# Kernel optimization log

Measured on AMD Instinct MI355X. Metric: run time of the kernel, lower is better.

## Reference

```python
import jax, jax.numpy as jnp
import numpy as np

BEV_H, BEV_W = 496, 432  # cfg.bevshape

def mish(x):
    return x * jnp.tanh(jax.nn.softplus(x))

def ln(x, g, b, eps=1e-5):
    m = jnp.mean(x, axis=-1, keepdims=True)
    v = jnp.mean((x - m) ** 2, axis=-1, keepdims=True)
    return (x - m) * jax.lax.rsqrt(v + eps) * g + b

def fel(x, W, g, b):
    # FELayer: Linear(bias=False) -> LayerNorm -> Mish
    return mish(ln(x @ W.T, g, b))

def setup_inputs() -> dict:
    key = jax.random.key(0)
    ks = iter(jax.random.split(key, 48))
    Nv, P, Cin, Cv, Nb = 16000, 32, 10, 64, 16000
    inp = {}
    inp['voxels'] = jax.random.normal(next(ks), (Nv, P, Cin), jnp.float32)
    inp['voxelmask'] = jax.random.bernoulli(next(ks), 0.7, (Nv, P, 1)).astype(jnp.float32)
    inp['bevsidx'] = jax.random.randint(next(ks), (Nb, 64), 0, Nv, dtype=jnp.int32)
    flat = jax.random.choice(next(ks), BEV_H * BEV_W, (Nb,), replace=False)
    inp['bevcoors'] = jnp.stack([flat // BEV_W, flat % BEV_W], axis=1).astype(jnp.int32)
    inp['bevmask'] = jax.random.bernoulli(next(ks), 0.8, (Nb, 1, 1)).astype(jnp.float32)
    def w(shape):
        return jax.random.normal(next(ks), shape, jnp.float32) * 0.05
    for i, cin in zip((1, 2, 3, 4), (Cin, Cv, Cv, Cv)):
        inp[f'vfe{i}_W'] = w((Cv, cin))
        inp[f'vfe{i}_g'] = jnp.ones((Cv,), jnp.float32)
        inp[f'vfe{i}_b'] = jnp.zeros((Cv,), jnp.float32)
    inp['bfe1_W'] = w((16, Cv, Cv));  inp['bfe1_g'] = jnp.ones((16, Cv));  inp['bfe1_b'] = jnp.zeros((16, Cv))
    inp['bfe2a_W'] = w((16, 8, Cv)); inp['bfe2a_g'] = jnp.ones((16, 8));  inp['bfe2a_b'] = jnp.zeros((16, 8))
    inp['bfe2b_W'] = w((16, 8, 32)); inp['bfe2b_g'] = jnp.ones((16, 8));  inp['bfe2b_b'] = jnp.zeros((16, 8))
    inp['bfe3_W'] = w((128, 128));   inp['bfe3_g'] = jnp.ones((128,));   inp['bfe3_b'] = jnp.zeros((128,))
    return inp

def reference(voxels, voxelmask, bevsidx, bevcoors, bevmask,
              vfe1_W, vfe1_g, vfe1_b, vfe2_W, vfe2_g, vfe2_b,
              vfe3_W, vfe3_g, vfe3_b, vfe4_W, vfe4_g, vfe4_b,
              bfe1_W, bfe1_g, bfe1_b, bfe2a_W, bfe2a_g, bfe2a_b,
              bfe2b_W, bfe2b_g, bfe2b_b, bfe3_W, bfe3_g, bfe3_b):
    # voxel feature encoder with masked residual
    x1 = fel(voxels, vfe1_W, vfe1_g, vfe1_b)            # [Nv, P, 64]
    x2 = fel(x1, vfe2_W, vfe2_g, vfe2_b) * voxelmask
    x3 = fel(x2, vfe3_W, vfe3_g, vfe3_b)
    x4 = fel(x3, vfe4_W, vfe4_g, vfe4_b) * voxelmask + x2
    voxelwise = jnp.max(x4, axis=1)                     # [Nv, 64]
    # gather 64 voxels per BEV cell
    bevs = voxelwise[bevsidx]                           # [Nb, 64 voxels, 64 ch]
    x0 = jnp.transpose(bevs, (0, 2, 1))                 # [Nb, 64 ch, 64 voxels]
    Nb = x0.shape[0]
    xg = x0.reshape(Nb, 16, 4, 64)                      # 16 branches of 4 channel-rows
    # bfe1_k (vectorized over the 16 branches) + bev mask
    h = mish(ln(jnp.einsum('ngpc,goc->ngpo', xg, bfe1_W), bfe1_g[:, None, :], bfe1_b[:, None, :]))
    h = h * bevmask[:, None]                            # bevmask [Nb,1,1] -> broadcast
    # bfe2_k: NormalFELayer(in_points=4, in=64, out=8)
    h = mish(ln(jnp.einsum('ngpc,goc->ngpo', h, bfe2a_W), bfe2a_g[:, None, :], bfe2a_b[:, None, :]))
    h = h.reshape(Nb, 16, 32)
    h = mish(ln(jnp.einsum('ngc,goc->ngo', h, bfe2b_W), bfe2b_g, bfe2b_b))  # [Nb,16,8]
    x17 = h.reshape(Nb, 128)                            # cat of 16 branches
    x18 = fel(x17, bfe3_W, bfe3_g, bfe3_b)
    x19 = fel(x18, bfe3_W, bfe3_g, bfe3_b) + x17        # same bfe3 applied twice + residual
    bevmap = jnp.zeros((BEV_H, BEV_W, 128), jnp.float32).at[bevcoors[:, 0], bevcoors[:, 1]].set(x19)
    return jnp.transpose(bevmap, (2, 1, 0))             # [128, W, H]
```

## Files before the change

### kernel.cpp

```cpp
#include <hip/hip_runtime.h>
#include <math.h>

constexpr int NV  = 16000;
constexpr int P   = 32;
constexpr int CIN = 10;
constexpr int CV  = 64;
constexpr int NB  = 16000;
constexpr int BEV_H = 496, BEV_W = 432;
constexpr int HW = BEV_H * BEV_W;
constexpr float EPS = 1e-5f;

typedef __attribute__((ext_vector_type(8))) short short8_t;
typedef __attribute__((ext_vector_type(4))) short short4_t;
typedef __attribute__((ext_vector_type(4))) float fx4;
typedef __attribute__((ext_vector_type(2))) float f32x2;

__device__ __forceinline__ float mish(float x) {
  float e = __expf(fminf(x, 15.f));
  float u = 1.f + e;
  float d = fmaf(u, u, 1.f);
  float r = __builtin_amdgcn_rcpf(d);
  return fmaf(-2.f * x, r, x);
}

__device__ __forceinline__ short f2bf(float f) {
  unsigned u = __builtin_bit_cast(unsigned, f);
  u += 0x7FFF + ((u >> 16) & 1);
  return (short)(u >> 16);
}
__device__ __forceinline__ float bf2f(short s) {
  unsigned u = ((unsigned)(unsigned short)s) << 16;
  return __builtin_bit_cast(float, u);
}
__device__ __forceinline__ short8_t pack8(const float* t) {
  short8_t s;
#pragma unroll
  for (int j = 0; j < 8; ++j) s[j] = f2bf(t[j]);
  return s;
}

__device__ __forceinline__ unsigned bfpair(float a, float b) {
  unsigned au = __builtin_bit_cast(unsigned, a) + 0x8000u;
  unsigned bu = __builtin_bit_cast(unsigned, b) + 0x8000u;
  return __builtin_amdgcn_perm(bu, au, 0x07060302u);
}
__device__ __forceinline__ unsigned hipack(float a, float b, float& la, float& lb) {
  unsigned ua = (__builtin_bit_cast(unsigned, a) + 0x8000u) & 0xFFFF0000u;
  unsigned ub = (__builtin_bit_cast(unsigned, b) + 0x8000u) & 0xFFFF0000u;
  la = a - __builtin_bit_cast(float, ua);
  lb = b - __builtin_bit_cast(float, ub);
  return __builtin_amdgcn_perm(ub, ua, 0x07060302u);
}

__global__ __launch_bounds__(256) void pack_weights_kernel(
    const float* __restrict__ W1, const float* __restrict__ W2a,
    const float* __restrict__ W2b, const float* __restrict__ W3,
    short* __restrict__ w1h,
    short* __restrict__ w2ah,
    short* __restrict__ w2bh,
    short* __restrict__ w3h, short* __restrict__ w3l)
{
  int i = blockIdx.x * 256 + threadIdx.x;
  if (i < 65536) {
    w1h[i] = f2bf(W1[i]);
  } else if (i < 81920) {
    int j = i - 65536;
    int g = j >> 10, o = (j >> 6) & 15, c = j & 63;
    float v = (o < 8) ? W2a[(g * 8 + o) * 64 + c] : 0.f;
    w2ah[j] = f2bf(v);
  } else if (i < 90112) {
    int k = i - 81920;
    int g = k >> 9, o = (k >> 5) & 15, c = k & 31;
    float v = (o < 8) ? W2b[(g * 8 + o) * 32 + c] : 0.f;
    w2bh[k] = f2bf(v);
  } else if (i < 106496) {
    int j = i - 90112;
    float v = W3[j];
    short h = f2bf(v);
    w3h[j] = h; w3l[j] = f2bf(v - bf2f(h));
  }
}

__global__ __launch_bounds__(256, 4) void vfe_mfma5_kernel(
    const float* __restrict__ voxels, const float* __restrict__ vmask,
    const float* __restrict__ W1, const float* __restrict__ g1, const float* __restrict__ b1,
    const float* __restrict__ W2, const float* __restrict__ g2, const float* __restrict__ b2,
    const float* __restrict__ W3, const float* __restrict__ g3, const float* __restrict__ b3,
    const float* __restrict__ W4, const float* __restrict__ g4, const float* __restrict__ b4,
    unsigned short* __restrict__ voxelwise)
{
  __shared__ short wlds[28 * 512];
  __shared__ short actb[4][16 * 72];
  __shared__ float gblds[512];

  const int tid  = threadIdx.x;
  const int lane = tid & 63;
  const int w    = tid >> 6;
  const int p    = lane & 15;
  const int q    = lane >> 4;
  const int gw   = blockIdx.x * 4 + w;

  for (int k = tid; k < 512; k += 256) {
    int region = k >> 6, off = k & 63;
    const float* src =
        region == 0 ? g1 : region == 1 ? b1 :
        region == 2 ? g2 : region == 3 ? b2 :
        region == 4 ? g3 : region == 5 ? b3 :
        region == 6 ? g4 : b4;
    gblds[k] = src[off];
  }
  for (int s = w; s < 28; s += 4) {
    float t[8];
    if (s < 4) {
      const int f = s;
#pragma unroll
      for (int j = 0; j < 8; ++j) {
        int c = 8 * q + j;
        t[j] = (c < CIN) ? W1[(p + 16 * f) * CIN + c] : 0.f;
      }
    } else {
      const int l = (s - 4) >> 3, rem = (s - 4) & 7, ch = rem >> 2, f = rem & 3;
      const float* Wl = (l == 0) ? W2 : (l == 1) ? W3 : W4;
      const float* src = Wl + (p + 16 * f) * CV + 32 * ch + 8 * q;
#pragma unroll
      for (int j = 0; j < 8; ++j) t[j] = src[j];
    }
    *(short8_t*)&wlds[s * 512 + lane * 8] = pack8(t);
  }
  __syncthreads();

  short* mybuf = &actb[w][0];
  const fx4 zacc = {0.f, 0.f, 0.f, 0.f};
  const int srcLane = ((lane >> 2) & 3) * 16 + (((lane >> 4) & 3) << 2) + (lane & 3);

  for (int i = 0; i < 4; ++i) {
    const int v = gw * 4 + i;
    float chmax0 = 0.f, vmaxv = 0.f;

    for (int h = 0; h < 2; ++h) {
      const int ptbase = v * 32 + h * 16;
      const float m = vmask[ptbase + p];
      float x2r[16];
      float cur[16];

      {
        const float* xrow = voxels + (size_t)(ptbase + p) * CIN;
        float t[8] = {0.f, 0.f, 0.f, 0.f, 0.f, 0.f, 0.f, 0.f};
        if (q == 0) {
          float2 a = *(const float2*)(xrow + 0);
          float2 b = *(const float2*)(xrow + 2);
          float2 c = *(const float2*)(xrow + 4);
          float2 d = *(const float2*)(xrow + 6);
          t[0] = a.x; t[1] = a.y; t[2] = b.x; t[3] = b.y;
          t[4] = c.x; t[5] = c.y; t[6] = d.x; t[7] = d.y;
        } else if (q == 1) {
          float2 a = *(const float2*)(xrow + 8);
          t[0] = a.x; t[1] = a.y;
        }
        uint4 bu = make_uint4(bfpair(t[0], t[1]), bfpair(t[2], t[3]),
                              bfpair(t[4], t[5]), bfpair(t[6], t[7]));
        short8_t bfrag = __builtin_bit_cast(short8_t, bu);
        fx4 acc[4];
#pragma unroll
        for (int f = 0; f < 4; ++f) {
          short8_t af = *(short8_t*)&wlds[f * 512 + lane * 8];
          acc[f] = __builtin_amdgcn_mfma_f32_16x16x32_bf16(af, bfrag, zacc, 0, 0, 0);
        }
        f32x2 s1v = {0.f, 0.f}, s2v = {0.f, 0.f};
#pragma unroll
        for (int f = 0; f < 4; ++f) {
          f32x2 a01 = __builtin_shufflevector(acc[f], acc[f], 0, 1);
          f32x2 a23 = __builtin_shufflevector(acc[f], acc[f], 2, 3);
          s1v = s1v + a01 + a23;
          s2v = __builtin_elementwise_fma(a01, a01, s2v);
          s2v = __builtin_elementwise_fma(a23, a23, s2v);
        }
        float s1 = s1v[0] + s1v[1], s2 = s2v[0] + s2v[1];
        s1 += __shfl_xor(s1, 16); s1 += __shfl_xor(s1, 32);
        s2 += __shfl_xor(s2, 16); s2 += __shfl_xor(s2, 32);
        float mean = s1 * (1.f / 64.f);
        float rstd = rsqrtf(fmaf(-mean, mean, s2 * (1.f / 64.f)) + EPS);
        float ms = -mean * rstd;
#pragma unroll
        for (int f = 0; f < 4; ++f) {
          float4 gv = *(const float4*)&gblds[16 * f + 4 * q];
          float4 bv = *(const float4*)&gblds[64 + 16 * f + 4 * q];
          float go[4] = {gv.x, gv.y, gv.z, gv.w};
          float bo[4] = {bv.x, bv.y, bv.z, bv.w};
          float o[4];
#pragma unroll
          for (int r = 0; r < 4; ++r)
            o[r] = mish(fmaf(fmaf(acc[f][r], rstd, ms), go[r], bo[r]));
          *(uint2*)&mybuf[p * 72 + 4 * q + 16 * f] =
              make_uint2(bfpair(o[0], o[1]), bfpair(o[2], o[3]));
        }
      }

#pragma unroll 1
      for (int l = 0; l < 3; ++l) {
        short8_t bf0 = *(short8_t*)&mybuf[p * 72 + 8 * q];
        short8_t bf1 = *(short8_t*)&mybuf[p * 72 + 8 * q + 32];
        fx4 acc[4];
#pragma unroll
        for (int f = 0; f < 4; ++f) {
          short8_t a0 = *(short8_t*)&wlds[(4 + l * 8 + f) * 512 + lane * 8];
          short8_t a1 = *(short8_t*)&wlds[(4 + l * 8 + 4 + f) * 512 + lane * 8];
          fx4 a = __builtin_amdgcn_mfma_f32_16x16x32_bf16(a0, bf0, zacc, 0, 0, 0);
          acc[f] = __builtin_amdgcn_mfma_f32_16x16x32_bf16(a1, bf1, a, 0, 0, 0);
        }
        f32x2 s1v = {0.f, 0.f}, s2v = {0.f, 0.f};
#pragma unroll
        for (int f = 0; f < 4; ++f) {
          f32x2 a01 = __builtin_shufflevector(acc[f], acc[f], 0, 1);
          f32x2 a23 = __builtin_shufflevector(acc[f], acc[f], 2, 3);
          s1v = s1v + a01 + a23;
          s2v = __builtin_elementwise_fma(a01, a01, s2v);
          s2v = __builtin_elementwise_fma(a23, a23, s2v);
        }
        float s1 = s1v[0] + s1v[1], s2 = s2v[0] + s2v[1];
        s1 += __shfl_xor(s1, 16); s1 += __shfl_xor(s1, 32);
        s2 += __shfl_xor(s2, 16); s2 += __shfl_xor(s2, 32);
        float mean = s1 * (1.f / 64.f);
        float rstd = rsqrtf(fmaf(-mean, mean, s2 * (1.f / 64.f)) + EPS);
        float ms = -mean * rstd;
        const int gbbase = (l + 1) * 128;
#pragma unroll
        for (int f = 0; f < 4; ++f) {
          float4 gv = *(const float4*)&gblds[gbbase + 16 * f + 4 * q];
          float4 bv = *(const float4*)&gblds[gbbase + 64 + 16 * f + 4 * q];
          float go[4] = {gv.x, gv.y, gv.z, gv.w};
          float bo[4] = {bv.x, bv.y, bv.z, bv.w};
          if (l == 0) {
            float o[4];
#pragma unroll
            for (int r = 0; r < 4; ++r) {
              o[r] = mish(fmaf(fmaf(acc[f][r], rstd, ms), go[r], bo[r])) * m;
              x2r[f * 4 + r] = o[r];
            }
            *(uint2*)&mybuf[p * 72 + 4 * q + 16 * f] =
                make_uint2(bfpair(o[0], o[1]), bfpair(o[2], o[3]));
          } else if (l == 1) {
            float o[4];
#pragma unroll
            for (int r = 0; r < 4; ++r)
              o[r] = mish(fmaf(fmaf(acc[f][r], rstd, ms), go[r], bo[r]));
            *(uint2*)&mybuf[p * 72 + 4 * q + 16 * f] =
                make_uint2(bfpair(o[0], o[1]), bfpair(o[2], o[3]));
          } else {
#pragma unroll
            for (int r = 0; r < 4; ++r) {
              float t1 = fmaf(fmaf(acc[f][r], rstd, ms), go[r], bo[r]);
              cur[f * 4 + r] = fmaf(mish(t1), m, x2r[f * 4 + r]);
            }
          }
        }
      }

#pragma unroll
      for (int t = 0; t < 8; ++t) {
        float send = (lane & 8) ? cur[t] : cur[t + 8];
        float got  = __shfl_xor(send, 8);
        float mine = (lane & 8) ? cur[t + 8] : cur[t];
        cur[t] = fmaxf(mine, got);
      }
#pragma unroll
      for (int t = 0; t < 4; ++t) {
        float send = (lane & 4) ? cur[t] : cur[t + 4];
        float got  = __shfl_xor(send, 4);
        float mine = (lane & 4) ? cur[t + 4] : cur[t];
        cur[t] = fmaxf(mine, got);
      }
#pragma unroll
      for (int t = 0; t < 2; ++t) {
        float send = (lane & 2) ? cur[t] : cur[t + 2];
        float got  = __shfl_xor(send, 2);
        float mine = (lane & 2) ? cur[t + 2] : cur[t];
        cur[t] = fmaxf(mine, got);
      }
      {
        float send = (lane & 1) ? cur[0] : cur[1];
        float got  = __shfl_xor(send, 1);
        float mine = (lane & 1) ? cur[1] : cur[0];
        cur[0] = fmaxf(mine, got);
      }
      float hm = __shfl(cur[0], srcLane);
      if (h == 0) chmax0 = hm; else vmaxv = fmaxf(chmax0, hm);
    }
    unsigned uv = __builtin_bit_cast(unsigned, vmaxv) + 0x8000u;
    voxelwise[v * 64 + lane] = (unsigned short)(uv >> 16);
  }
}

constexpr int XS_CELL = 64 * 64 + 16;
constexpr int ACT_OFF = 4 * XS_CELL;
constexpr int ACT_WS  = 16 * 72;
constexpr int GB_OFF  = ACT_OFF + 8 * ACT_WS;
constexpr int GB_FLOATS = 2560;
constexpr int SMEM_SHORTS = GB_OFF + 2 * (GB_FLOATS + 4 * 132);

__device__ __forceinline__ uint2 gather_transpose(uint2 u2, int bit0, int bit1) {
  float a0 = __builtin_bit_cast(float, u2.x << 16);
  float a1 = __builtin_bit_cast(float, u2.x & 0xFFFF0000u);
  float a2 = __builtin_bit_cast(float, u2.y << 16);
  float a3 = __builtin_bit_cast(float, u2.y & 0xFFFF0000u);
  float gv0 = bit0 ? a0 : a1, gv1 = bit0 ? a2 : a3;
  float r0 = __shfl_xor(gv0, 4), r1 = __shfl_xor(gv1, 4);
  float c0 = bit0 ? r0 : a0, c1 = bit0 ? a1 : r0;
  float c2 = bit0 ? r1 : a2, c3 = bit0 ? a3 : r1;
  float h0 = bit1 ? c0 : c2, h1 = bit1 ? c1 : c3;
  float s0 = __shfl_xor(h0, 8), s1 = __shfl_xor(h1, 8);
  float d0 = bit1 ? s0 : c0, d1 = bit1 ? s1 : c1;
  float d2 = bit1 ? c2 : s0, d3 = bit1 ? c3 : s1;
  return make_uint2(bfpair(d0, d1), bfpair(d2, d3));
}

__global__ __launch_bounds__(512, 4) void bfe12_mfma8_kernel(
    const unsigned short* __restrict__ voxelwise, const int* __restrict__ bevsidx,
    const float* __restrict__ bevmask,
    const short* __restrict__ w1h,
    const float* __restrict__ g1, const float* __restrict__ b1,
    const short* __restrict__ w2ah,
    const float* __restrict__ g2a, const float* __restrict__ b2a,
    const short* __restrict__ w2bh,
    const float* __restrict__ g2b, const float* __restrict__ b2b,
    float* __restrict__ x17buf)
{
  __shared__ short sm[SMEM_SHORTS];
  float* gbf  = (float*)&sm[GB_OFF];
  float* x17f = gbf + GB_FLOATS;

  const int tid  = threadIdx.x;
  const int lane = tid & 63;
  const int w    = tid >> 6;
  const int r15  = lane & 15;
  const int q    = lane >> 4;
  const int cellbase = blockIdx.x * 4;

  const int chq   = lane & 3;
  const int v_loc = (lane >> 2) & 3;
  const int vblk  = lane >> 4;
  const int bit0  = v_loc & 1, bit1 = v_loc >> 1;
  const int gcell = w >> 1;
  const int vb0   = (w & 1) * 2;

  for (int k = tid; k < GB_FLOATS; k += 512) {
    float v;
    if (k < 1024)      v = g1[k];
    else if (k < 2048) v = b1[k - 1024];
    else if (k < 2176) v = g2a[k - 2048];
    else if (k < 2304) v = b2a[k - 2176];
    else if (k < 2432) v = g2b[k - 2304];
    else               v = b2b[k - 2432];
    gbf[k] = v;
  }

  int idxr[2];
#pragma unroll
  for (int vi = 0; vi < 2; ++vi)
    idxr[vi] = bevsidx[(cellbase + gcell) * 64 + 16 * (vb0 + vi) + 4 * vblk + v_loc];

  uint2 raw[2][4];
#pragma unroll
  for (int vi = 0; vi < 2; ++vi)
#pragma unroll
    for (int js = 0; js < 4; ++js)
      raw[vi][js] = *(const uint2*)(voxelwise + (size_t)idxr[vi] * 64 +
                                    16 * js + 4 * chq);
#pragma unroll
  for (int js = 0; js < 4; ++js)
#pragma unroll
    for (int vi = 0; vi < 2; ++vi) {
      uint2 packed = gather_transpose(raw[vi][js], bit0, bit1);
      const int vb    = vb0 + vi;
      const int ch    = 16 * js + 4 * chq + v_loc;
      const int chunk = (2 * vb + (vblk >> 1)) ^ (ch & 7);
      const int addr  = gcell * XS_CELL + ch * 64 + 8 * chunk + 4 * (vblk & 1);
      *(uint2*)&sm[addr] = packed;
    }

  __syncthreads();

  const fx4 zacc = {0.f, 0.f, 0.f, 0.f};
  short* acth = &sm[ACT_OFF + w * ACT_WS];
  short* h2h  = acth;
  const int cl = r15 >> 2, p = r15 & 3;
  const float bm = bevmask[cellbase + cl];

#pragma unroll
  for (int j = 0; j < 2; ++j) {
    const int g = 8 * j + w;

    short8_t W1f[2][4];
#pragma unroll
    for (int c = 0; c < 2; ++c)
#pragma unroll
      for (int f = 0; f < 4; ++f) {
        int off = (g * 64 + r15 + 16 * f) * 64 + 32 * c + 8 * q;
        W1f[c][f] = *(const short8_t*)&w1h[off];
      }
    short8_t W2af[2];
#pragma unroll
    for (int c = 0; c < 2; ++c) {
      int off = (g * 16 + r15) * 64 + 32 * c + 8 * q;
      W2af[c] = *(const short8_t*)&w2ah[off];
    }
    short8_t W2bf;
    {
      int off = (g * 16 + r15) * 32 + 8 * q;
      W2bf = *(const short8_t*)&w2bh[off];
    }

    {
      const int ch    = 4 * g + p;
      const int sw    = ch & 7;
      const int xbase = cl * XS_CELL + ch * 64;
      short8_t x0 = *(short8_t*)&sm[xbase + 8 * (q ^ sw)];
      short8_t x1 = *(short8_t*)&sm[xbase + 8 * ((4 + q) ^ sw)];

      fx4 acc[4];
#pragma unroll
      for (int f = 0; f < 4; ++f) {
        fx4 a = __builtin_amdgcn_mfma_f32_16x16x32_bf16(W1f[0][f], x0, zacc, 0, 0, 0);
        acc[f] = __builtin_amdgcn_mfma_f32_16x16x32_bf16(W1f[1][f], x1, a, 0, 0, 0);
      }

      f32x2 s1v = {0.f, 0.f}, s2v = {0.f, 0.f};
#pragma unroll
      for (int f = 0; f < 4; ++f) {
        f32x2 a01 = __builtin_shufflevector(acc[f], acc[f], 0, 1);
        f32x2 a23 = __builtin_shufflevector(acc[f], acc[f], 2, 3);
        s1v = s1v + a01 + a23;
        s2v = __builtin_elementwise_fma(a01, a01, s2v);
        s2v = __builtin_elementwise_fma(a23, a23, s2v);
      }
      float s1 = s1v[0] + s1v[1], s2 = s2v[0] + s2v[1];
      s1 += __shfl_xor(s1, 16); s1 += __shfl_xor(s1, 32);
      s2 += __shfl_xor(s2, 16); s2 += __shfl_xor(s2, 32);
      float mean = s1 * (1.f / 64.f);
      float rstd = rsqrtf(fmaf(-mean, mean, s2 * (1.f / 64.f)) + EPS);
      float ms = -mean * rstd;

#pragma unroll
      for (int f = 0; f < 4; ++f) {
        float4 gv = *(const float4*)&gbf[g * 64 + 16 * f + 4 * q];
        float4 bv = *(const float4*)&gbf[1024 + g * 64 + 16 * f + 4 * q];
        float go[4] = {gv.x, gv.y, gv.z, gv.w};
        float bo[4] = {bv.x, bv.y, bv.z, bv.w};
        float o[4];
#pragma unroll
        for (int r = 0; r < 4; ++r)
          o[r] = mish(fmaf(fmaf(acc[f][r], rstd, ms), go[r], bo[r])) * bm;
        *(uint2*)&acth[r15 * 72 + 16 * f + 4 * q] =
            make_uint2(bfpair(o[0], o[1]), bfpair(o[2], o[3]));
      }

      short8_t a0 = *(short8_t*)&acth[r15 * 72 + 8 * q];
      short8_t a1 = *(short8_t*)&acth[r15 * 72 + 32 + 8 * q];

      if (lane < 60) *(uint2*)&h2h[160 + 8 * lane] = make_uint2(0u, 0u);

      fx4 a2 = __builtin_amdgcn_mfma_f32_16x16x32_bf16(W2af[0], a0, zacc, 0, 0, 0);
      a2 = __builtin_amdgcn_mfma_f32_16x16x32_bf16(W2af[1], a1, a2, 0, 0, 0);

      float sa = a2[0] + a2[1] + a2[2] + a2[3];
      float sb = fmaf(a2[0], a2[0], fmaf(a2[1], a2[1], fmaf(a2[2], a2[2], a2[3] * a2[3])));
      sa += __shfl_xor(sa, 16); sb += __shfl_xor(sb, 16);
      if (q < 2) {
        float mean2 = sa * 0.125f;
        float rstd2 = rsqrtf(fmaf(-mean2, mean2, sb * 0.125f) + EPS);
        float ms2 = -mean2 * rstd2;
        float4 gv = *(const float4*)&gbf[2048 + g * 8 + 4 * q];
        float4 bv = *(const float4*)&gbf[2176 + g * 8 + 4 * q];
        float go[4] = {gv.x, gv.y, gv.z, gv.w};
        float bo[4] = {bv.x, bv.y, bv.z, bv.w};
        float o[4];
#pragma unroll
        for (int r = 0; r < 4; ++r)
          o[r] = mish(fmaf(fmaf(a2[r], rstd2, ms2), go[r], bo[r]));
        *(uint2*)&h2h[cl * 40 + p * 8 + 4 * q] =
            make_uint2(bfpair(o[0], o[1]), bfpair(o[2], o[3]));
      }
    }

    {
      short8_t bh = *(short8_t*)&h2h[r15 * 40 + 8 * q];
      fx4 a3 = __builtin_amdgcn_mfma_f32_16x16x32_bf16(W2bf, bh, zacc, 0, 0, 0);

      float sa = a3[0] + a3[1] + a3[2] + a3[3];
      float sb = fmaf(a3[0], a3[0], fmaf(a3[1], a3[1], fmaf(a3[2], a3[2], a3[3] * a3[3])));
      sa += __shfl_xor(sa, 16); sb += __shfl_xor(sb, 16);
      if (q < 2 && r15 < 4) {
        float mean3 = sa * 0.125f;
        float rstd3 = rsqrtf(fmaf(-mean3, mean3, sb * 0.125f) + EPS);
        float ms3 = -mean3 * rstd3;
        float4 gv = *(const float4*)&gbf[2304 + g * 8 + 4 * q];
        float4 bv = *(const float4*)&gbf[2432 + g * 8 + 4 * q];
        float go[4] = {gv.x, gv.y, gv.z, gv.w};
        float bo[4] = {bv.x, bv.y, bv.z, bv.w};
        float4 outv;
        float* op = &outv.x;
#pragma unroll
        for (int r = 0; r < 4; ++r)
          op[r] = mish(fmaf(fmaf(a3[r], rstd3, ms3), go[r], bo[r]));
        *(float4*)&x17f[r15 * 132 + g * 8 + 4 * q] = outv;
      }
    }
  }

  __syncthreads();
  if (tid < 128) {
    const int cell = tid >> 5;
    const int off  = (tid & 31) * 4;
    float4 vq = *(const float4*)&x17f[cell * 132 + off];
    *(float4*)&x17buf[(size_t)(cellbase + cell) * 128 + off] = vq;
  }
}

__global__ __launch_bounds__(256, 3) void bfe3_mfma2_kernel(
    const float* __restrict__ x17buf, const int* __restrict__ bevcoors,
    const short* __restrict__ w3h, const short* __restrict__ w3l,
    const float* __restrict__ g3, const float* __restrict__ b3,
    float* __restrict__ out)
{
  __shared__ short x18h[4][16 * 136];
  __shared__ short x18l[4][16 * 136];

  const int tid  = threadIdx.x;
  const int lane = tid & 63;
  const int w    = tid >> 6;
  const int r15  = lane & 15;
  const int q    = lane >> 4;
  const int cell = blockIdx.x * 64 + w * 16 + r15;
  const float* xr = x17buf + (size_t)cell * 128;
  short* xh18 = &x18h[w][0];
  short* xl18 = &x18l[w][0];
  const fx4 zacc = {0.f, 0.f, 0.f, 0.f};

  short8_t xh[4], xl[4];
#pragma unroll
  for (int c = 0; c < 4; ++c) {
    const float* s = xr + 32 * c + 8 * q;
    float4 A = *(const float4*)s;
    float4 B = *(const float4*)(s + 4);
    float t[8] = {A.x, A.y, A.z, A.w, B.x, B.y, B.z, B.w};
    unsigned hu[4], lu[4];
#pragma unroll
    for (int jj = 0; jj < 4; ++jj) {
      float la, lb;
      hu[jj] = hipack(t[2 * jj], t[2 * jj + 1], la, lb);
      lu[jj] = bfpair(la, lb);
    }
    xh[c] = __builtin_bit_cast(short8_t, make_uint4(hu[0], hu[1], hu[2], hu[3]));
    xl[c] = __builtin_bit_cast(short8_t, make_uint4(lu[0], lu[1], lu[2], lu[3]));
  }

  fx4 acc[8];
#pragma unroll
  for (int f = 0; f < 8; ++f) {
    fx4 a = zacc;
#pragma unroll
    for (int c = 0; c < 4; ++c) {
      int off = (16 * f + r15) * 128 + 32 * c + 8 * q;
      short8_t Ah = *(const short8_t*)&w3h[off];
      short8_t Al = *(const short8_t*)&w3l[off];
      a = __builtin_amdgcn_mfma_f32_16x16x32_bf16(Ah, xh[c], a, 0, 0, 0);
      a = __builtin_amdgcn_mfma_f32_16x16x32_bf16(Ah, xl[c], a, 0, 0, 0);
      a = __builtin_amdgcn_mfma_f32_16x16x32_bf16(Al, xh[c], a, 0, 0, 0);
    }
    acc[f] = a;
  }
  {
    f32x2 s1v = {0.f, 0.f}, s2v = {0.f, 0.f};
#pragma unroll
    for (int f = 0; f < 8; ++f) {
      f32x2 a01 = __builtin_shufflevector(acc[f], acc[f], 0, 1);
      f32x2 a23 = __builtin_shufflevector(acc[f], acc[f], 2, 3);
      s1v = s1v + a01 + a23;
      s2v = __builtin_elementwise_fma(a01, a01, s2v);
      s2v = __builtin_elementwise_fma(a23, a23, s2v);
    }
    float s1 = s1v[0] + s1v[1], s2 = s2v[0] + s2v[1];
    s1 += __shfl_xor(s1, 16); s1 += __shfl_xor(s1, 32);
    s2 += __shfl_xor(s2, 16); s2 += __shfl_xor(s2, 32);
    float mean = s1 * (1.f / 128.f);
    float rstd = rsqrtf(fmaf(-mean, mean, s2 * (1.f / 128.f)) + EPS);
    float ms = -mean * rstd;
#pragma unroll
    for (int f = 0; f < 8; ++f) {
      float4 gv = *(const float4*)(g3 + 16 * f + 4 * q);
      float4 bv = *(const float4*)(b3 + 16 * f + 4 * q);
      float go[4] = {gv.x, gv.y, gv.z, gv.w};
      float bo[4] = {bv.x, bv.y, bv.z, bv.w};
      float o[4];
#pragma unroll
      for (int r = 0; r < 4; ++r)
        o[r] = mish(fmaf(fmaf(acc[f][r], rstd, ms), go[r], bo[r]));
      float la0, lb0, la1, lb1;
      unsigned h01 = hipack(o[0], o[1], la0, lb0);
      unsigned h23 = hipack(o[2], o[3], la1, lb1);
      *(uint2*)&xh18[r15 * 136 + 16 * f + 4 * q] = make_uint2(h01, h23);
      *(uint2*)&xl18[r15 * 136 + 16 * f + 4 * q] =
          make_uint2(bfpair(la0, lb0), bfpair(la1, lb1));
    }
  }

  short8_t yh[4], yl[4];
#pragma unroll
  for (int c = 0; c < 4; ++c) {
    yh[c] = *(short8_t*)&xh18[r15 * 136 + 32 * c + 8 * q];
    yl[c] = *(short8_t*)&xl18[r15 * 136 + 32 * c + 8 * q];
  }
#pragma unroll
  for (int f = 0; f < 8; ++f) {
    fx4 a = zacc;
#pragma unroll
    for (int c = 0; c < 4; ++c) {
      int off = (16 * f + r15) * 128 + 32 * c + 8 * q;
      short8_t Ah = *(const short8_t*)&w3h[off];
      short8_t Al = *(const short8_t*)&w3l[off];
      a = __builtin_amdgcn_mfma_f32_16x16x32_bf16(Ah, yh[c], a, 0, 0, 0);
      a = __builtin_amdgcn_mfma_f32_16x16x32_bf16(Ah, yl[c], a, 0, 0, 0);
      a = __builtin_amdgcn_mfma_f32_16x16x32_bf16(Al, yh[c], a, 0, 0, 0);
    }
    acc[f] = a;
  }
  {
    f32x2 s1v = {0.f, 0.f}, s2v = {0.f, 0.f};
#pragma unroll
    for (int f = 0; f < 8; ++f) {
      f32x2 a01 = __builtin_shufflevector(acc[f], acc[f], 0, 1);
      f32x2 a23 = __builtin_shufflevector(acc[f], acc[f], 2, 3);
      s1v = s1v + a01 + a23;
      s2v = __builtin_elementwise_fma(a01, a01, s2v);
      s2v = __builtin_elementwise_fma(a23, a23, s2v);
    }
    float s1 = s1v[0] + s1v[1], s2 = s2v[0] + s2v[1];
    s1 += __shfl_xor(s1, 16); s1 += __shfl_xor(s1, 32);
    s2 += __shfl_xor(s2, 16); s2 += __shfl_xor(s2, 32);
    float mean = s1 * (1.f / 128.f);
    float rstd = rsqrtf(fmaf(-mean, mean, s2 * (1.f / 128.f)) + EPS);
    float ms = -mean * rstd;

    int2 hw2 = *(const int2*)&bevcoors[cell * 2];
    const int base = hw2.y * BEV_H + hw2.x;
#pragma unroll
    for (int f = 0; f < 8; ++f) {
      float4 gv = *(const float4*)(g3 + 16 * f + 4 * q);
      float4 bv = *(const float4*)(b3 + 16 * f + 4 * q);
      float go[4] = {gv.x, gv.y, gv.z, gv.w};
      float bo[4] = {bv.x, bv.y, bv.z, bv.w};
      float4 R = *(const float4*)(xr + 16 * f + 4 * q);
      float Ra[4] = {R.x, R.y, R.z, R.w};
#pragma unroll
      for (int r = 0; r < 4; ++r) {
        float t1 = fmaf(fmaf(acc[f][r], rstd, ms), go[r], bo[r]);
        float val = mish(t1) + Ra[r];
        out[(size_t)(16 * f + 4 * q + r) * HW + base] = val;
      }
    }
  }
}

extern "C" void kernel_launch(void* const* d_in, const int* in_sizes, int n_in,
                              void* d_out, int out_size, void* d_ws, size_t ws_size,
                              hipStream_t stream) {
  const float* voxels   = (const float*)d_in[0];
  const float* vmask    = (const float*)d_in[1];
  const int*   bevsidx  = (const int*)d_in[2];
  const int*   bevcoors = (const int*)d_in[3];
  const float* bevmask  = (const float*)d_in[4];
  const float* vfe1_W = (const float*)d_in[5];
  const float* vfe1_g = (const float*)d_in[6];
  const float* vfe1_b = (const float*)d_in[7];
  const float* vfe2_W = (const float*)d_in[8];
  const float* vfe2_g = (const float*)d_in[9];
  const float* vfe2_b = (const float*)d_in[10];
  const float* vfe3_W = (const float*)d_in[11];
  const float* vfe3_g = (const float*)d_in[12];
  const float* vfe3_b = (const float*)d_in[13];
  const float* vfe4_W = (const float*)d_in[14];
  const float* vfe4_g = (const float*)d_in[15];
  const float* vfe4_b = (const float*)d_in[16];
  const float* bfe1_W  = (const float*)d_in[17];
  const float* bfe1_g  = (const float*)d_in[18];
  const float* bfe1_b  = (const float*)d_in[19];
  const float* bfe2a_W = (const float*)d_in[20];
  const float* bfe2a_g = (const float*)d_in[21];
  const float* bfe2a_b = (const float*)d_in[22];
  const float* bfe2b_W = (const float*)d_in[23];
  const float* bfe2b_g = (const float*)d_in[24];
  const float* bfe2b_b = (const float*)d_in[25];
  const float* bfe3_W  = (const float*)d_in[26];
  const float* bfe3_g  = (const float*)d_in[27];
  const float* bfe3_b  = (const float*)d_in[28];

  unsigned short* voxelwise = (unsigned short*)d_ws;
  float* x17buf = (float*)(voxelwise + (size_t)NV * 64);
  short* wbase  = (short*)(x17buf + (size_t)NB * 128);
  short* w1h  = wbase;
  short* w2ah = w1h + 65536;
  short* w2bh = w2ah + 16384;
  short* w3h  = w2bh + 8192;
  short* w3l  = w3h + 16384;
  float* out = (float*)d_out;

  hipMemsetAsync(d_out, 0, (size_t)out_size * sizeof(float), stream);

  pack_weights_kernel<<<(106496 + 255) / 256, 256, 0, stream>>>(
      bfe1_W, bfe2a_W, bfe2b_W, bfe3_W,
      w1h, w2ah, w2bh, w3h, w3l);

  vfe_mfma5_kernel<<<NV / 16, 256, 0, stream>>>(
      voxels, vmask,
      vfe1_W, vfe1_g, vfe1_b, vfe2_W, vfe2_g, vfe2_b,
      vfe3_W, vfe3_g, vfe3_b, vfe4_W, vfe4_g, vfe4_b,
      voxelwise);

  bfe12_mfma8_kernel<<<NB / 4, 512, 0, stream>>>(
      voxelwise, bevsidx, bevmask,
      w1h, bfe1_g, bfe1_b,
      w2ah, bfe2a_g, bfe2a_b,
      w2bh, bfe2b_g, bfe2b_b,
      x17buf);

  bfe3_mfma2_kernel<<<NB / 64, 256, 0, stream>>>(
      x17buf, bevcoors, w3h, w3l, bfe3_g, bfe3_b, out);
}
```

Baseline: 418.2 us.

## Replace memset plus scattered output writes with inverse-map dense expand kernel

Instead of zeroing the whole 128xWxH output and then scattering each cell's 128 channels with strided single-float stores, bfe3 now writes compact per-cell rows. A new expand kernel walks every BEV pixel, looks up its source cell through an inverse map built in the weight-pack kernel, and writes coalesced rows (zeros where there is no cell) via an LDS transpose. This trades the memset and uncoalesced scatter for an extra 8 MB compact buffer round-trip, an HW-sized int map memset, and one more launch. Duplicate coordinates would now resolve by a nondeterministic write order in the map.

```diff
diff --git a/kernel.cpp b/kernel.cpp
--- a/kernel.cpp
+++ b/kernel.cpp
@@ -55,12 +55,18 @@
 __global__ __launch_bounds__(256) void pack_weights_kernel(
     const float* __restrict__ W1, const float* __restrict__ W2a,
     const float* __restrict__ W2b, const float* __restrict__ W3,
+    const int* __restrict__ bevcoors,
     short* __restrict__ w1h,
     short* __restrict__ w2ah,
     short* __restrict__ w2bh,
-    short* __restrict__ w3h, short* __restrict__ w3l)
+    short* __restrict__ w3h, short* __restrict__ w3l,
+    int* __restrict__ invmap)
 {
   int i = blockIdx.x * 256 + threadIdx.x;
+  if (i < NB) {
+    int2 hw2 = *(const int2*)&bevcoors[i * 2];
+    invmap[hw2.y * BEV_H + hw2.x] = i;
+  }
   if (i < 65536) {
     w1h[i] = f2bf(W1[i]);
   } else if (i < 81920) {
@@ -516,11 +522,11 @@
   }
 }
 
-__global__ __launch_bounds__(256, 3) void bfe3_mfma2_kernel(
-    const float* __restrict__ x17buf, const int* __restrict__ bevcoors,
+__global__ __launch_bounds__(256, 3) void bfe3_mfma3_kernel(
+    const float* __restrict__ x17buf,
     const short* __restrict__ w3h, const short* __restrict__ w3l,
     const float* __restrict__ g3, const float* __restrict__ b3,
-    float* __restrict__ out)
+    float* __restrict__ x19c)
 {
   __shared__ short x18h[4][16 * 136];
   __shared__ short x18l[4][16 * 136];
@@ -641,8 +647,6 @@
     float rstd = rsqrtf(fmaf(-mean, mean, s2 * (1.f / 128.f)) + EPS);
     float ms = -mean * rstd;
 
-    int2 hw2 = *(const int2*)&bevcoors[cell * 2];
-    const int base = hw2.y * BEV_H + hw2.x;
 #pragma unroll
     for (int f = 0; f < 8; ++f) {
       float4 gv = *(const float4*)(g3 + 16 * f + 4 * q);
@@ -651,13 +655,47 @@
       float bo[4] = {bv.x, bv.y, bv.z, bv.w};
       float4 R = *(const float4*)(xr + 16 * f + 4 * q);
       float Ra[4] = {R.x, R.y, R.z, R.w};
+      float4 ov;
+      float* op = &ov.x;
 #pragma unroll
       for (int r = 0; r < 4; ++r) {
         float t1 = fmaf(fmaf(acc[f][r], rstd, ms), go[r], bo[r]);
-        float val = mish(t1) + Ra[r];
-        out[(size_t)(16 * f + 4 * q + r) * HW + base] = val;
-      }
-    }
+        op[r] = mish(t1) + Ra[r];
+      }
+      *(float4*)&x19c[(size_t)cell * 128 + 16 * f + 4 * q] = ov;
+    }
+  }
+}
+
+__global__ __launch_bounds__(256) void expand_kernel(
+    const float* __restrict__ x19c, const int* __restrict__ invmap,
+    float* __restrict__ out)
+{
+  __shared__ float tile[64][133];
+  const int tid   = threadIdx.x;
+  const int pbase = blockIdx.x * 64;
+  const int r     = tid & 63;
+  const int part  = tid >> 6;
+  const int cell  = invmap[pbase + r];
+  if (cell >= 0) {
+    const float* src = x19c + (size_t)cell * 128 + part * 32;
+#pragma unroll
+    for (int k = 0; k < 8; ++k) {
+      float4 v = *(const float4*)(src + 4 * k);
+      tile[r][part * 32 + 4 * k + 0] = v.x;
+      tile[r][part * 32 + 4 * k + 1] = v.y;
+      tile[r][part * 32 + 4 * k + 2] = v.z;
+      tile[r][part * 32 + 4 * k + 3] = v.w;
+    }
+  } else {
+#pragma unroll
+    for (int k = 0; k < 32; ++k) tile[r][part * 32 + k] = 0.f;
+  }
+  __syncthreads();
+#pragma unroll
+  for (int cc = 0; cc < 32; ++cc) {
+    const int c = part * 32 + cc;
+    out[(size_t)c * HW + pbase + r] = tile[r][c];
   }
 }
 
@@ -696,7 +734,9 @@
 
   unsigned short* voxelwise = (unsigned short*)d_ws;
   float* x17buf = (float*)(voxelwise + (size_t)NV * 64);
-  short* wbase  = (short*)(x17buf + (size_t)NB * 128);
+  float* x19c   = x17buf + (size_t)NB * 128;
+  int*   invmap = (int*)(x19c + (size_t)NB * 128);
+  short* wbase  = (short*)(invmap + HW);
   short* w1h  = wbase;
   short* w2ah = w1h + 65536;
   short* w2bh = w2ah + 16384;
@@ -704,11 +744,11 @@
   short* w3l  = w3h + 16384;
   float* out = (float*)d_out;
 
-  hipMemsetAsync(d_out, 0, (size_t)out_size * sizeof(float), stream);
+  hipMemsetAsync(invmap, 0xFF, (size_t)HW * sizeof(int), stream);
 
   pack_weights_kernel<<<(106496 + 255) / 256, 256, 0, stream>>>(
-      bfe1_W, bfe2a_W, bfe2b_W, bfe3_W,
-      w1h, w2ah, w2bh, w3h, w3l);
+      bfe1_W, bfe2a_W, bfe2b_W, bfe3_W, bevcoors,
+      w1h, w2ah, w2bh, w3h, w3l, invmap);
 
   vfe_mfma5_kernel<<<NV / 16, 256, 0, stream>>>(
       voxels, vmask,
@@ -723,6 +763,8 @@
       w2bh, bfe2b_g, bfe2b_b,
       x17buf);
 
-  bfe3_mfma2_kernel<<<NB / 64, 256, 0, stream>>>(
-      x17buf, bevcoors, w3h, w3l, bfe3_g, bfe3_b, out);
-}
+  bfe3_mfma3_kernel<<<NB / 64, 256, 0, stream>>>(
+      x17buf, w3h, w3l, bfe3_g, bfe3_b, x19c);
+
+  expand_kernel<<<HW / 64, 256, 0, stream>>>(x19c, invmap, out);
+}
```

Result: faster. 402.5 us (-3.8%).
